# Kernel tuning notes

Measured on AMD Instinct MI355X. Metric: run time of the kernel, lower is better.

## Reference

```python
import jax, jax.numpy as jnp
import numpy as np

N_NODES = 20000   # atoms
N_EDGES = 300000  # directed edges within cutoff
N_TRIP = 500000   # triplets (k->j->i)
H = 128           # hidden_channels
NR = 6            # num_radial
NS = 7            # num_spherical
NB = 8            # num_bilinear
OUT = 128         # out_channels
NLAY = 3          # num_layers in OutputBlock
NOB = 2           # num_blocks + 1 output blocks


def _silu(v):
    return v * jax.nn.sigmoid(v)  # swish


def setup_inputs() -> dict:
    key = jax.random.key(0)
    ks = jax.random.split(key, 20)
    s = lambda fan: np.float32(1.0 / np.sqrt(fan))
    inp = {}
    inp["x"] = jax.random.normal(ks[0], (N_EDGES, H), jnp.float32)
    inp["rbf"] = jax.random.uniform(ks[1], (N_EDGES, NR), jnp.float32)
    inp["sbf"] = jax.random.uniform(ks[2], (N_TRIP, NS * NR), jnp.float32)
    inp["i"] = jax.random.randint(ks[3], (N_EDGES,), 0, N_NODES)
    inp["idx_kj"] = jax.random.randint(ks[4], (N_TRIP,), 0, N_EDGES)
    inp["idx_ji"] = jax.random.randint(ks[5], (N_TRIP,), 0, N_EDGES)
    # Interaction params (weights stored [in, out] so y = x @ W)
    inp["W_rbf"] = jax.random.normal(ks[6], (NR, H), jnp.float32) * s(NR)
    inp["W_sbf"] = jax.random.normal(ks[7], (NS * NR, NB), jnp.float32) * s(NS * NR)
    inp["W_kj"] = jax.random.normal(ks[8], (H, H), jnp.float32) * s(H)
    inp["b_kj"] = jnp.zeros((H,), jnp.float32)
    inp["W_ji"] = jax.random.normal(ks[9], (H, H), jnp.float32) * s(H)
    inp["b_ji"] = jnp.zeros((H,), jnp.float32)
    inp["W_bil"] = jax.random.normal(ks[10], (H, NB, H), jnp.float32) * np.float32(2.0 / H)
    inp["W_lin"] = jax.random.normal(ks[11], (H, H), jnp.float32) * s(H)
    inp["b_lin"] = jnp.zeros((H,), jnp.float32)
    # OutputBlock params, stacked over the NOB blocks
    inp["out_lin_rbf"] = jax.random.normal(ks[12], (NOB, NR, H), jnp.float32) * s(NR)
    inp["out_lins_W"] = jax.random.normal(ks[13], (NOB, NLAY, H, H), jnp.float32) * s(H)
    inp["out_lins_b"] = jnp.zeros((NOB, NLAY, H), jnp.float32)
    inp["out_lin"] = jax.random.normal(ks[14], (NOB, H, OUT), jnp.float32) * s(H)
    return inp


def _output_block(xe, rbf, i, lin_rbf, lins_W, lins_b, lin_out):
    # OutputBlock.forward: gate edge features by rbf projection, scatter to nodes
    g = (rbf @ lin_rbf) * xe              # [E, H]
    g = jax.ops.segment_sum(g, i, num_segments=N_NODES)  # [N, H]
    for li in range(NLAY):
        g = _silu(g @ lins_W[li] + lins_b[li])
    return g @ lin_out                    # [N, OUT]


def _interaction(x, rbf, sbf, idx_kj, idx_ji,
                 W_rbf, W_sbf, W_kj, b_kj, W_ji, b_ji, W_bil, W_lin, b_lin):
    r = rbf @ W_rbf                       # [E, H]
    sproj = sbf @ W_sbf                   # [T, NB]
    x_ji = _silu(x @ W_ji + b_ji)         # [E, H]
    x_kj = _silu(x @ W_kj + b_kj) * r     # [E, H]
    xg = x_kj[idx_kj]                     # [T, H] triplet gather
    # einsum('wj,wl,ijl->wi', sproj, xg, W_bil) without the [T, H, NB] blowup:
    # loop over the small fixed bilinear dim NB, accumulating [T, H]
    t = jnp.zeros((xg.shape[0], H), xg.dtype)
    for jb in range(NB):
        t = t + sproj[:, jb:jb + 1] * (xg @ W_bil[:, jb, :].T)
    agg = jax.ops.segment_sum(t, idx_ji, num_segments=N_EDGES)  # scatter to edges
    return _silu((x_ji + agg) @ W_lin + b_lin)


def reference(x, rbf, sbf, i, idx_kj, idx_ji,
              W_rbf, W_sbf, W_kj, b_kj, W_ji, b_ji, W_bil, W_lin, b_lin,
              out_lin_rbf, out_lins_W, out_lins_b, out_lin):
    P = _output_block(x, rbf, i, out_lin_rbf[0], out_lins_W[0], out_lins_b[0], out_lin[0])
    x2 = _interaction(x, rbf, sbf, idx_kj, idx_ji,
                      W_rbf, W_sbf, W_kj, b_kj, W_ji, b_ji, W_bil, W_lin, b_lin)
    P = P + _output_block(x2, rbf, i, out_lin_rbf[1], out_lins_W[1], out_lins_b[1], out_lin[1])
    return P.sum(axis=0)  # batch=None path: global readout [OUT]
```

## Files before the change

### kernel.cpp

```cpp
#include <hip/hip_runtime.h>
#include <hip/hip_fp16.h>

#define NN 20000
#define NE 300000
#define NT 500000
#define HD 128
#define NRR 6
#define NSNRD 42
#define NBB 8

using f16x8 = __attribute__((ext_vector_type(8))) _Float16;
using f32x4 = __attribute__((ext_vector_type(4))) float;

__device__ __forceinline__ float silu_f(float v){ return v / (1.f + __expf(-v)); }

__device__ __forceinline__ void pk_add(__half2* p, float lo, float hi){
  __half2 h = __floats2half2_rn(lo, hi);
  unsigned int b = *reinterpret_cast<unsigned int*>(&h);
  asm volatile("global_atomic_pk_add_f16 %0, %1, off" :: "v"(p), "v"(b) : "memory");
}

__device__ __forceinline__ void gload16(const void* g, char* lds_dst){
  __builtin_amdgcn_global_load_lds(
    (const __attribute__((address_space(1))) void*)g,
    (__attribute__((address_space(3))) void*)lds_dst, 16, 0, 0);
}

__global__ void k_x16(const float* __restrict__ x, __half* __restrict__ xh){
  long i = ((long)blockIdx.x*256 + threadIdx.x)*8;
  if(i < (long)NE*HD){
    float4 a = *(const float4*)(x+i), b = *(const float4*)(x+i+4);
    __half h8[8];
    h8[0]=__float2half(a.x); h8[1]=__float2half(a.y);
    h8[2]=__float2half(a.z); h8[3]=__float2half(a.w);
    h8[4]=__float2half(b.x); h8[5]=__float2half(b.y);
    h8[6]=__float2half(b.z); h8[7]=__float2half(b.w);
    *(float4*)(xh+i) = *(float4*)h8;
  }
}

__global__ void k_prep(const float* __restrict__ Wb, __half* __restrict__ WB2,
                       const float* __restrict__ Wkj, const float* __restrict__ Wji,
                       const float* __restrict__ Wlin, __half* __restrict__ WkjT,
                       __half* __restrict__ WjiT, __half* __restrict__ WlinT,
                       const float* __restrict__ olW, __half* __restrict__ wo6){
  int bid = blockIdx.x, tid = threadIdx.x;
  if(bid < 512){
    int idx = bid*256 + tid;
    int l = idx & 127, i = (idx>>7) & 127, jb = idx>>14;
    WB2[jb*16384 + i*128 + l] = __float2half(Wb[i*1024 + jb*128 + l]);
  } else if(bid < 704){
    int idx = (bid-512)*256 + tid;
    int which = idx>>14, rem = idx & 16383;
    int i = rem>>7, k = rem & 127;
    const float* src = which==0 ? Wkj : (which==1 ? Wji : Wlin);
    __half* dst = which==0 ? WkjT : (which==1 ? WjiT : WlinT);
    dst[rem] = __float2half(src[k*HD + i]);
  } else {
    int idx = (bid-704)*256 + tid;
    int lw = idx>>14, rem = idx & 16383;
    int i = rem>>7, k = rem & 127;
    wo6[lw*16384 + rem] = __float2half(olW[lw*16384 + k*HD + i]);
  }
}

#define EROWS 128
#define PRE_A 0
#define PRE_B 32768
#define PRE_RBF 65536
#define PRE_WR 68608
#define PRE_LS 71680
#define PRE_NID 74752
#define SH_PRE 75264
__global__ __launch_bounds__(512,4)
void k_edge_pre(const __half* __restrict__ xh, const float* __restrict__ rbf,
                const int* __restrict__ nid, const __half* __restrict__ WkjT,
                const float* __restrict__ bkj, const float* __restrict__ Wrbf,
                const float* __restrict__ lrbf0, __half* __restrict__ xkj,
                __half* __restrict__ g0){
  extern __shared__ char sm[];
  int tid = threadIdx.x;
  long e0 = (long)blockIdx.x * EROWS;
  for(int c=tid;c<2048;c+=512){
    int i=c>>4, cc=c&15;
    float4 v = *(const float4*)(WkjT + i*128 + cc*8);
    *(float4*)(sm + PRE_B + ((i*256+cc*16)^((i&7)<<4))) = v;
  }
  for(int c=tid;c<2048;c+=512){
    int r=c>>4, cc=c&15; long e=e0+r;
    float4 v = (e<NE) ? *(const float4*)(xh + e*HD + cc*8)
                      : (float4){0.f,0.f,0.f,0.f};
    *(float4*)(sm + PRE_A + ((r*256+cc*16)^((r&7)<<4))) = v;
  }
  float* rbft=(float*)(sm+PRE_RBF);
  for(int q=tid;q<EROWS*NRR;q+=512){ long e=e0+q/NRR; rbft[q]=(e<NE)? rbf[e*NRR + q%NRR] : 0.f; }
  float* wrbf=(float*)(sm+PRE_WR);
  for(int q=tid;q<NRR*HD;q+=512) wrbf[q]=Wrbf[q];
  float* ls0=(float*)(sm+PRE_LS);
  for(int q=tid;q<NRR*HD;q+=512) ls0[q]=lrbf0[q];
  int* nids=(int*)(sm+PRE_NID);
  if (tid < EROWS){ long e=e0+tid; nids[tid]=(e<NE)? nid[e] : 0; }
  __syncthreads();
  int lane=tid&63, wid=tid>>6, wr=wid>>1, wc=wid&1;
  f16x8 af[2][4];
  #pragma unroll
  for(int rt=0;rt<2;rt++){
    int r = wr*32 + rt*16 + (lane&15);
    #pragma unroll
    for(int ks=0;ks<4;ks++)
      af[rt][ks] = *(const f16x8*)(sm + PRE_A + ((r*256 + (ks*4+(lane>>4))*16)^((r&7)<<4)));
  }
  f32x4 acc[2][4];
  #pragma unroll
  for(int rt=0;rt<2;rt++){
    #pragma unroll
    for(int ct=0;ct<4;ct++) acc[rt][ct]=(f32x4){0.f,0.f,0.f,0.f};
  }
  #pragma unroll
  for(int ct=0;ct<4;ct++){
    int i = wc*64 + ct*16 + (lane&15);
    #pragma unroll
    for(int ks=0;ks<4;ks++){
      f16x8 b = *(const f16x8*)(sm + PRE_B + ((i*256 + (ks*4+(lane>>4))*16)^((i&7)<<4)));
      acc[0][ct] = __builtin_amdgcn_mfma_f32_16x16x32_f16(af[0][ks], b, acc[0][ct], 0,0,0);
      acc[1][ct] = __builtin_amdgcn_mfma_f32_16x16x32_f16(af[1][ks], b, acc[1][ct], 0,0,0);
    }
  }
  #pragma unroll
  for(int rt=0;rt<2;rt++){
    #pragma unroll
    for(int j=0;j<4;j++){
      int rloc = wr*32 + rt*16 + (lane>>4)*4 + j;
      long e = e0 + rloc;
      bool ok = (e<NE);
      int nb = nids[rloc];
      #pragma unroll
      for(int ct=0;ct<4;ct++){
        int h = wc*64 + ct*16 + (lane&15);
        float v = silu_f(acc[rt][ct][j] + bkj[h]);
        float r2=0.f, gate=0.f;
        #pragma unroll
        for(int q=0;q<NRR;q++){
          float rb = rbft[rloc*NRR+q];
          r2   += rb*wrbf[q*HD+h];
          gate += rb*ls0[q*HD+h];
        }
        float xval = __half2float(*(const __half*)(sm + PRE_A +
                       ((rloc*256 + (h>>3)*16)^((rloc&7)<<4)) + (h&7)*2));
        float w1 = v*r2;
        float w2 = gate*xval;
        float p1 = __shfl_xor(w1, 1, 64);
        float p2 = __shfl_xor(w2, 1, 64);
        if(ok && !(lane&1)){
          *(__half2*)(xkj + e*HD + h) = __floats2half2_rn(w1, p1);
          pk_add((__half2*)(g0 + (long)nb*HD + h), w2, p2);
        }
      }
    }
  }
}

#define TROWS 128
#define OFF_BUF 0
#define OFF_SP 49152
#define OFF_KJ 51200
#define OFF_JI 51712
#define OFF_WSB 52224
#define SH_TRIP 53568
__global__ __launch_bounds__(512,4)
void k_triplet_mfma(const __half* __restrict__ xkj, const float* __restrict__ sbf,
                    const float* __restrict__ Wsbf,
                    const int* __restrict__ ikj, const int* __restrict__ iji,
                    const __half* __restrict__ WB2, __half* __restrict__ agg){
  extern __shared__ char sm[];
  int tid = threadIdx.x;
  long t0 = (long)blockIdx.x * TROWS;
  int* kjs = (int*)(sm + OFF_KJ);
  int* jis = (int*)(sm + OFF_JI);
  if (tid < TROWS){
    int ok = (t0 + tid) < NT;
    kjs[tid] = ok ? ikj[t0+tid] : 0;
    jis[tid] = ok ? iji[t0+tid] : -1;
  }
  float* sbuf = (float*)(sm + OFF_BUF);
  for(int q=tid;q<TROWS*NSNRD;q+=512){
    long t = t0 + q/NSNRD;
    sbuf[q] = (t<NT) ? sbf[t*NSNRD + q%NSNRD] : 0.f;
  }
  float* wsb = (float*)(sm + OFF_WSB);
  for(int q=tid;q<NSNRD*NBB;q+=512) wsb[q]=Wsbf[q];
  __syncthreads();
  __half* spl = (__half*)(sm + OFF_SP);
  {
    int r = tid>>2, j0 = (tid&3)*2;
    float a0=0.f,a1=0.f;
    for(int q=0;q<NSNRD;q++){
      float v = sbuf[r*NSNRD+q];
      a0 += v*wsb[q*NBB+j0];
      a1 += v*wsb[q*NBB+j0+1];
    }
    spl[r*NBB+j0]=__float2half(a0); spl[r*NBB+j0+1]=__float2half(a1);
  }
  __syncthreads();
  for(int c=tid;c<TROWS*16;c+=512){
    int w = c>>4, cc = c&15;
    float4 v = *(const float4*)(xkj + (long)kjs[w]*HD + cc*8);
    *(float4*)(sm + OFF_BUF + ((w*256 + cc*16)^((w&7)<<4))) = v;
  }
  __syncthreads();
  int lane = tid & 63;
  int wid = tid>>6, wr = wid>>1, wc = wid&1;
  f16x8 au[2][4];
  #pragma unroll
  for(int rt=0;rt<2;rt++){
    int w = wr*32 + rt*16 + (lane&15);
    #pragma unroll
    for(int ks=0;ks<4;ks++)
      au[rt][ks] = *(const f16x8*)(sm + OFF_BUF + ((w*256 + ks*64 + (lane>>4)*16)^((w&7)<<4)));
  }
  __syncthreads();
  #pragma unroll
  for(int u=0;u<2;u++){
    int c = u*512 + tid;
    int i = c>>3, lc = (c&7) ^ (i&7);
    gload16(WB2 + i*128 + lc*8,
            sm + OFF_BUF + u*8192 + (tid>>6)*1024);
  }
  #pragma unroll
  for(int u=0;u<2;u++){
    int c = u*512 + tid;
    int i = c>>3, lc = (c&7) ^ (i&7);
    gload16(WB2 + i*128 + 64 + lc*8,
            sm + OFF_BUF + 16384 + u*8192 + (tid>>6)*1024);
  }
  f32x4 acc[2][4];
  #pragma unroll
  for(int rt=0;rt<2;rt++){
    #pragma unroll
    for(int ct=0;ct<4;ct++) acc[rt][ct] = (f32x4){0.f,0.f,0.f,0.f};
  }
  _Float16 sr[2];
  #pragma unroll
  for(int p=0;p<16;p++){
    int jb = p>>1, h = p&1;
    if(h==0){
      #pragma unroll
      for(int rt=0;rt<2;rt++)
        sr[rt] = *(const _Float16*)&spl[(wr*32 + rt*16 + (lane&15))*NBB + jb];
    }
    if(p<15) asm volatile("s_waitcnt vmcnt(2)" ::: "memory");
    else     asm volatile("s_waitcnt vmcnt(0)" ::: "memory");
    __builtin_amdgcn_s_barrier();
    asm volatile("" ::: "memory");
    if(p+2 < 16){
      int np = p+2, njb = np>>1, nh = np&1;
      #pragma unroll
      for(int u=0;u<2;u++){
        int c = u*512 + tid;
        int i = c>>3, lc = (c&7) ^ (i&7);
        gload16(WB2 + njb*16384 + i*128 + nh*64 + lc*8,
                sm + OFF_BUF + ((p+2)%3)*16384 + u*8192 + (tid>>6)*1024);
      }
    }
    const char* bbase = sm + OFF_BUF + (p%3)*16384;
    #pragma unroll
    for(int ksl=0;ksl<2;ksl++){
      int ks = h*2 + ksl;
      f16x8 as2[2];
      #pragma unroll
      for(int rt=0;rt<2;rt++){
        #pragma unroll
        for(int j=0;j<8;j++) as2[rt][j] = au[rt][ks][j]*sr[rt];
      }
      #pragma unroll
      for(int ct=0;ct<4;ct++){
        int it = wc*64 + ct*16 + (lane&15);
        int chunk = (ksl*4 + (lane>>4)) ^ (it&7);
        f16x8 b = *(const f16x8*)(bbase + it*128 + chunk*16);
        #pragma unroll
        for(int rt=0;rt<2;rt++)
          acc[rt][ct] = __builtin_amdgcn_mfma_f32_16x16x32_f16(as2[rt], b, acc[rt][ct], 0,0,0);
      }
    }
  }
  #pragma unroll
  for(int rt=0;rt<2;rt++){
    #pragma unroll
    for(int r=0;r<4;r++){
      int w = wr*32 + rt*16 + (lane>>4)*4 + r;
      int ji = jis[w];
      #pragma unroll
      for(int ct=0;ct<4;ct++){
        float v = acc[rt][ct][r];
        float p = __shfl_xor(v, 1, 64);
        if (ji >= 0 && !(lane&1))
          pk_add((__half2*)(agg + (long)ji*HD + wc*64 + ct*16 + (lane&15)), v, p);
      }
    }
  }
}

#define PO_A 0
#define PO_B 32768
#define PO_RBF 65536
#define PO_LS 68608
#define PO_NID 71680
#define SH_POST 72192
__global__ __launch_bounds__(512,4)
void k_edge_post(const __half* __restrict__ xh, const float* __restrict__ rbf,
                 const __half* __restrict__ aggh, const int* __restrict__ nid,
                 const __half* __restrict__ WjiT, const float* __restrict__ bji,
                 const __half* __restrict__ WlinT, const float* __restrict__ blin,
                 const float* __restrict__ lrbf1, __half* __restrict__ g1){
  extern __shared__ char sm[];
  int tid = threadIdx.x;
  long e0 = (long)blockIdx.x * EROWS;
  for(int c=tid;c<2048;c+=512){
    int i=c>>4, cc=c&15;
    float4 v = *(const float4*)(WjiT + i*128 + cc*8);
    *(float4*)(sm + PO_B + ((i*256+cc*16)^((i&7)<<4))) = v;
  }
  for(int c=tid;c<2048;c+=512){
    int r=c>>4, cc=c&15; long e=e0+r;
    float4 v = (e<NE) ? *(const float4*)(xh + e*HD + cc*8)
                      : (float4){0.f,0.f,0.f,0.f};
    *(float4*)(sm + PO_A + ((r*256+cc*16)^((r&7)<<4))) = v;
  }
  float* rbft=(float*)(sm+PO_RBF);
  for(int q=tid;q<EROWS*NRR;q+=512){ long e=e0+q/NRR; rbft[q]=(e<NE)? rbf[e*NRR + q%NRR] : 0.f; }
  float* ls1=(float*)(sm+PO_LS);
  for(int q=tid;q<NRR*HD;q+=512) ls1[q]=lrbf1[q];
  int* nids=(int*)(sm+PO_NID);
  if (tid < EROWS){ long e=e0+tid; nids[tid]=(e<NE)? nid[e] : 0; }
  __syncthreads();
  int lane=tid&63, wid=tid>>6, wr=wid>>1, wc=wid&1;
  f16x8 af[2][4];
  #pragma unroll
  for(int rt=0;rt<2;rt++){
    int r = wr*32 + rt*16 + (lane&15);
    #pragma unroll
    for(int ks=0;ks<4;ks++)
      af[rt][ks] = *(const f16x8*)(sm + PO_A + ((r*256 + (ks*4+(lane>>4))*16)^((r&7)<<4)));
  }
  f32x4 acc[2][4];
  #pragma unroll
  for(int rt=0;rt<2;rt++){
    #pragma unroll
    for(int ct=0;ct<4;ct++) acc[rt][ct]=(f32x4){0.f,0.f,0.f,0.f};
  }
  #pragma unroll
  for(int ct=0;ct<4;ct++){
    int i = wc*64 + ct*16 + (lane&15);
    #pragma unroll
    for(int ks=0;ks<4;ks++){
      f16x8 b = *(const f16x8*)(sm + PO_B + ((i*256 + (ks*4+(lane>>4))*16)^((i&7)<<4)));
      acc[0][ct] = __builtin_amdgcn_mfma_f32_16x16x32_f16(af[0][ks], b, acc[0][ct], 0,0,0);
      acc[1][ct] = __builtin_amdgcn_mfma_f32_16x16x32_f16(af[1][ks], b, acc[1][ct], 0,0,0);
    }
  }
  __syncthreads();
  #pragma unroll
  for(int rt=0;rt<2;rt++){
    #pragma unroll
    for(int j=0;j<4;j++){
      int rloc = wr*32 + rt*16 + (lane>>4)*4 + j;
      long e = e0 + rloc;
      #pragma unroll
      for(int ct=0;ct<4;ct++){
        int h = wc*64 + ct*16 + (lane&15);
        float v = silu_f(acc[rt][ct][j] + bji[h]);
        v += (e<NE) ? __half2float(aggh[e*HD + h]) : 0.f;
        int byo = ((rloc*256 + (h>>3)*16)^((rloc&7)<<4)) + (h&7)*2;
        *(__half*)(sm + PO_A + byo) = __float2half(v);
      }
    }
  }
  for(int c=tid;c<2048;c+=512){
    int i=c>>4, cc=c&15;
    float4 v = *(const float4*)(WlinT + i*128 + cc*8);
    *(float4*)(sm + PO_B + ((i*256+cc*16)^((i&7)<<4))) = v;
  }
  __syncthreads();
  f16x8 af2[2][4];
  #pragma unroll
  for(int rt=0;rt<2;rt++){
    int r = wr*32 + rt*16 + (lane&15);
    #pragma unroll
    for(int ks=0;ks<4;ks++)
      af2[rt][ks] = *(const f16x8*)(sm + PO_A + ((r*256 + (ks*4+(lane>>4))*16)^((r&7)<<4)));
  }
  f32x4 acc2[2][4];
  #pragma unroll
  for(int rt=0;rt<2;rt++){
    #pragma unroll
    for(int ct=0;ct<4;ct++) acc2[rt][ct]=(f32x4){0.f,0.f,0.f,0.f};
  }
  #pragma unroll
  for(int ct=0;ct<4;ct++){
    int i = wc*64 + ct*16 + (lane&15);
    #pragma unroll
    for(int ks=0;ks<4;ks++){
      f16x8 b = *(const f16x8*)(sm + PO_B + ((i*256 + (ks*4+(lane>>4))*16)^((i&7)<<4)));
      acc2[0][ct] = __builtin_amdgcn_mfma_f32_16x16x32_f16(af2[0][ks], b, acc2[0][ct], 0,0,0);
      acc2[1][ct] = __builtin_amdgcn_mfma_f32_16x16x32_f16(af2[1][ks], b, acc2[1][ct], 0,0,0);
    }
  }
  #pragma unroll
  for(int rt=0;rt<2;rt++){
    #pragma unroll
    for(int j=0;j<4;j++){
      int rloc = wr*32 + rt*16 + (lane>>4)*4 + j;
      long e = e0 + rloc;
      bool ok = (e<NE);
      int nb = nids[rloc];
      #pragma unroll
      for(int ct=0;ct<4;ct++){
        int h = wc*64 + ct*16 + (lane&15);
        float x2 = silu_f(acc2[rt][ct][j] + blin[h]);
        float gate = 0.f;
        #pragma unroll
        for(int q=0;q<NRR;q++) gate += rbft[rloc*NRR+q]*ls1[q*HD+h];
        float w = gate*x2;
        float p = __shfl_xor(w, 1, 64);
        if(ok && !(lane&1))
          pk_add((__half2*)(g1 + (long)nb*HD + h), w, p);
      }
    }
  }
}

#define SH_MLPC 65536
__global__ __launch_bounds__(512,4)
void k_mlp_chain(const __half* __restrict__ g0, const __half* __restrict__ g1,
                 const __half* __restrict__ wo6, const float* __restrict__ olb,
                 float* __restrict__ s0, float* __restrict__ s1){
  extern __shared__ char sm[];
  int tid = threadIdx.x;
  int nblk = (NN+EROWS-1)/EROWS;
  int which = blockIdx.x / nblk;
  long r0 = (long)(blockIdx.x % nblk) * EROWS;
  const __half* gin = which ? g1 : g0;
  float* s = which ? s1 : s0;
  for(int c=tid;c<2048;c+=512){
    int r=c>>4, cc=c&15; long rr=r0+r;
    float4 v;
    if(rr<NN) v = *(const float4*)(gin + rr*HD + cc*8);
    else      v = (float4){0.f,0.f,0.f,0.f};
    *(float4*)(sm + ((r*256+cc*16)^((r&7)<<4))) = v;
  }
  int lane=tid&63, wid=tid>>6, wr=wid>>1, wc=wid&1;
  for(int L=0; L<3; ++L){
    const __half* WT = wo6 + (which*3+L)*16384;
    const float* b   = olb + (which*3+L)*128;
    for(int c=tid;c<2048;c+=512){
      int i=c>>4, cc=c&15;
      float4 v = *(const float4*)(WT + i*128 + cc*8);
      *(float4*)(sm + 32768 + ((i*256+cc*16)^((i&7)<<4))) = v;
    }
    __syncthreads();
    f16x8 af[2][4];
    #pragma unroll
    for(int rt=0;rt<2;rt++){
      int r = wr*32 + rt*16 + (lane&15);
      #pragma unroll
      for(int ks=0;ks<4;ks++)
        af[rt][ks] = *(const f16x8*)(sm + ((r*256 + (ks*4+(lane>>4))*16)^((r&7)<<4)));
    }
    f32x4 acc[2][4];
    #pragma unroll
    for(int rt=0;rt<2;rt++){
      #pragma unroll
      for(int ct=0;ct<4;ct++) acc[rt][ct]=(f32x4){0.f,0.f,0.f,0.f};
    }
    #pragma unroll
    for(int ct=0;ct<4;ct++){
      int i = wc*64 + ct*16 + (lane&15);
      #pragma unroll
      for(int ks=0;ks<4;ks++){
        f16x8 bfr = *(const f16x8*)(sm + 32768 + ((i*256 + (ks*4+(lane>>4))*16)^((i&7)<<4)));
        acc[0][ct] = __builtin_amdgcn_mfma_f32_16x16x32_f16(af[0][ks], bfr, acc[0][ct], 0,0,0);
        acc[1][ct] = __builtin_amdgcn_mfma_f32_16x16x32_f16(af[1][ks], bfr, acc[1][ct], 0,0,0);
      }
    }
    __syncthreads();
    if(L < 2){
      #pragma unroll
      for(int rt=0;rt<2;rt++){
        #pragma unroll
        for(int j=0;j<4;j++){
          int rloc = wr*32 + rt*16 + (lane>>4)*4 + j;
          #pragma unroll
          for(int ct=0;ct<4;ct++){
            int h = wc*64 + ct*16 + (lane&15);
            float v = silu_f(acc[rt][ct][j] + b[h]);
            int byo = ((rloc*256 + (h>>3)*16)^((rloc&7)<<4)) + (h&7)*2;
            *(__half*)(sm + byo) = __float2half(v);
          }
        }
      }
    } else {
      float vsum[4];
      #pragma unroll
      for(int ct=0;ct<4;ct++) vsum[ct]=0.f;
      #pragma unroll
      for(int rt=0;rt<2;rt++){
        #pragma unroll
        for(int j=0;j<4;j++){
          int rloc = wr*32 + rt*16 + (lane>>4)*4 + j;
          long rr = r0 + rloc;
          #pragma unroll
          for(int ct=0;ct<4;ct++){
            int h = wc*64 + ct*16 + (lane&15);
            float v = (rr<NN) ? silu_f(acc[rt][ct][j] + b[h]) : 0.f;
            vsum[ct] += v;
          }
        }
      }
      #pragma unroll
      for(int ct=0;ct<4;ct++){
        vsum[ct] += __shfl_xor(vsum[ct], 16, 64);
        vsum[ct] += __shfl_xor(vsum[ct], 32, 64);
      }
      if((lane>>4)==0){
        #pragma unroll
        for(int ct=0;ct<4;ct++)
          atomicAdd(&s[wc*64 + ct*16 + (lane&15)], vsum[ct]);
      }
    }
  }
}

__global__ void k_readout(const float* __restrict__ s0, const float* __restrict__ s1,
                          const float* __restrict__ OL, float* __restrict__ out){
  int o = threadIdx.x;
  float acc=0.f;
  for(int h=0;h<HD;h++) acc += s0[h]*OL[h*HD+o] + s1[h]*OL[HD*HD + h*HD+o];
  out[o] = acc;
}

extern "C" void kernel_launch(void* const* d_in, const int* in_sizes, int n_in,
                              void* d_out, int out_size, void* d_ws, size_t ws_size,
                              hipStream_t stream) {
  const float* x     = (const float*)d_in[0];
  const float* rbf   = (const float*)d_in[1];
  const float* sbf   = (const float*)d_in[2];
  const int*   nid   = (const int*)d_in[3];
  const int*   ikj   = (const int*)d_in[4];
  const int*   iji   = (const int*)d_in[5];
  const float* W_rbf = (const float*)d_in[6];
  const float* W_sbf = (const float*)d_in[7];
  const float* W_kj  = (const float*)d_in[8];
  const float* b_kj  = (const float*)d_in[9];
  const float* W_ji  = (const float*)d_in[10];
  const float* b_ji  = (const float*)d_in[11];
  const float* W_bil = (const float*)d_in[12];
  const float* W_lin = (const float*)d_in[13];
  const float* b_lin = (const float*)d_in[14];
  const float* olrbf = (const float*)d_in[15];
  const float* olW   = (const float*)d_in[16];
  const float* olb   = (const float*)d_in[17];
  const float* olin  = (const float*)d_in[18];
  float* out = (float*)d_out;

  size_t off = 0;
  auto alloc = [&](size_t bytes)->size_t{ size_t r = off; off = (off + bytes + 255) & ~(size_t)255; return r; };
  size_t o_xkj  = alloc((size_t)NE*HD*2);
  size_t o_xh   = alloc((size_t)NE*HD*2);
  size_t o_agg  = alloc((size_t)NE*HD*2);
  size_t o_wb2  = alloc((size_t)NBB*HD*HD*2);
  size_t o_wkjT = alloc((size_t)HD*HD*2);
  size_t o_wjiT = alloc((size_t)HD*HD*2);
  size_t o_wlinT= alloc((size_t)HD*HD*2);
  size_t o_wo6  = alloc((size_t)6*HD*HD*2);
  size_t o_g0   = alloc((size_t)NN*HD*2);
  size_t o_g1   = alloc((size_t)NN*HD*2);
  size_t o_s0   = alloc(512);
  size_t o_s1   = alloc(512);
  if (off > ws_size) return;
  char* ws = (char*)d_ws;
  __half* xkj  = (__half*)(ws + o_xkj);
  __half* xh   = (__half*)(ws + o_xh);
  __half* agg  = (__half*)(ws + o_agg);
  __half* wb2  = (__half*)(ws + o_wb2);
  __half* wkjT = (__half*)(ws + o_wkjT);
  __half* wjiT = (__half*)(ws + o_wjiT);
  __half* wlinT= (__half*)(ws + o_wlinT);
  __half* wo6  = (__half*)(ws + o_wo6);
  __half* g0   = (__half*)(ws + o_g0);
  __half* g1   = (__half*)(ws + o_g1);
  float* s0    = (float*)(ws + o_s0);
  float* s1    = (float*)(ws + o_s1);

  hipFuncSetAttribute((const void*)k_edge_pre,     hipFuncAttributeMaxDynamicSharedMemorySize, SH_PRE);
  hipFuncSetAttribute((const void*)k_edge_post,    hipFuncAttributeMaxDynamicSharedMemorySize, SH_POST);
  hipFuncSetAttribute((const void*)k_triplet_mfma, hipFuncAttributeMaxDynamicSharedMemorySize, SH_TRIP);
  hipFuncSetAttribute((const void*)k_mlp_chain,    hipFuncAttributeMaxDynamicSharedMemorySize, SH_MLPC);

  hipMemsetAsync(agg, 0, (size_t)NE*HD*2, stream);
  hipMemsetAsync(g0,  0, (size_t)NN*HD*2, stream);
  hipMemsetAsync(g1,  0, (size_t)NN*HD*2, stream);
  hipMemsetAsync(s0,  0, 512, stream);
  hipMemsetAsync(s1,  0, 512, stream);

  k_x16<<<(int)(((long)NE*HD/8 + 255)/256),256,0,stream>>>(x, xh);
  k_prep<<<1088,256,0,stream>>>(W_bil, wb2, W_kj, W_ji, W_lin, wkjT, wjiT, wlinT, olW, wo6);

  k_edge_pre<<<(NE+EROWS-1)/EROWS,512,SH_PRE,stream>>>(xh, rbf, nid, wkjT, b_kj, W_rbf,
                                                       olrbf, xkj, g0);
  k_triplet_mfma<<<(NT+TROWS-1)/TROWS,512,SH_TRIP,stream>>>(xkj, sbf, W_sbf, ikj, iji, wb2, agg);
  k_edge_post<<<(NE+EROWS-1)/EROWS,512,SH_POST,stream>>>(xh, rbf, agg, nid, wjiT, b_ji,
                                                         wlinT, b_lin, olrbf + NRR*HD, g1);

  int mlpg = (NN+EROWS-1)/EROWS;
  k_mlp_chain<<<2*mlpg,512,SH_MLPC,stream>>>(g0, g1, wo6, olb, s0, s1);

  k_readout<<<1,128,0,stream>>>(s0, s1, olin, out);
}
```

Before: 736.7 us.

## Compute rbf projections with MFMA and load x tile directly from global

The two 6-wide rbf projections (r = rbf@W_rbf and gate = rbf@lin_rbf0) move from scalar FMA loops over LDS to fp16 MFMA, using K padded with zeros and fp16 copies of rbf and the weights staged in LDS. The x tile no longer goes through LDS: MFMA A fragments load straight from global memory, and the epilogue rereads x elements from global. This cuts LDS use and per-element scalar work, which may allow more resident blocks. It costs fp16 rounding of rbf and the weights, wasted MFMA work on the padded K, and scattered uncoalesced global reads of x in the epilogue.

New measurement: 763.6 us. +3.6%, slower.

```diff
diff --git a/kernel.cpp b/kernel.cpp
--- a/kernel.cpp
+++ b/kernel.cpp
@@ -65,13 +65,12 @@
 }
 
 #define EROWS 128
-#define PRE_A 0
-#define PRE_B 32768
-#define PRE_RBF 65536
-#define PRE_WR 68608
-#define PRE_LS 71680
-#define PRE_NID 74752
-#define SH_PRE 75264
+#define PRE_B 0
+#define PRE_RBF 32768
+#define PRE_WR 43008
+#define PRE_LS 53248
+#define PRE_NID 63488
+#define SH_PRE 64000
 __global__ __launch_bounds__(512,4)
 void k_edge_pre(const __half* __restrict__ xh, const float* __restrict__ rbf,
                 const int* __restrict__ nid, const __half* __restrict__ WkjT,
@@ -86,18 +85,18 @@
     float4 v = *(const float4*)(WkjT + i*128 + cc*8);
     *(float4*)(sm + PRE_B + ((i*256+cc*16)^((i&7)<<4))) = v;
   }
-  for(int c=tid;c<2048;c+=512){
-    int r=c>>4, cc=c&15; long e=e0+r;
-    float4 v = (e<NE) ? *(const float4*)(xh + e*HD + cc*8)
-                      : (float4){0.f,0.f,0.f,0.f};
-    *(float4*)(sm + PRE_A + ((r*256+cc*16)^((r&7)<<4))) = v;
-  }
-  float* rbft=(float*)(sm+PRE_RBF);
-  for(int q=tid;q<EROWS*NRR;q+=512){ long e=e0+q/NRR; rbft[q]=(e<NE)? rbf[e*NRR + q%NRR] : 0.f; }
-  float* wrbf=(float*)(sm+PRE_WR);
-  for(int q=tid;q<NRR*HD;q+=512) wrbf[q]=Wrbf[q];
-  float* ls0=(float*)(sm+PRE_LS);
-  for(int q=tid;q<NRR*HD;q+=512) ls0[q]=lrbf0[q];
+  __half* rbfp = (__half*)(sm + PRE_RBF);
+  for(int c=tid;c<4096;c+=512){
+    int r=c>>5, k=c&31; long e=e0+r;
+    rbfp[r*40+k] = (k<NRR && e<NE) ? __float2half(rbf[e*NRR+k]) : __float2half(0.f);
+  }
+  __half* wrt = (__half*)(sm + PRE_WR);
+  __half* lst = (__half*)(sm + PRE_LS);
+  for(int c=tid;c<4096;c+=512){
+    int i=c>>5, k=c&31;
+    wrt[i*40+k] = (k<NRR) ? __float2half(Wrbf[k*HD+i])  : __float2half(0.f);
+    lst[i*40+k] = (k<NRR) ? __float2half(lrbf0[k*HD+i]) : __float2half(0.f);
+  }
   int* nids=(int*)(sm+PRE_NID);
   if (tid < EROWS){ long e=e0+tid; nids[tid]=(e<NE)? nid[e] : 0; }
   __syncthreads();
@@ -105,16 +104,19 @@
   f16x8 af[2][4];
   #pragma unroll
   for(int rt=0;rt<2;rt++){
-    int r = wr*32 + rt*16 + (lane&15);
-    #pragma unroll
-    for(int ks=0;ks<4;ks++)
-      af[rt][ks] = *(const f16x8*)(sm + PRE_A + ((r*256 + (ks*4+(lane>>4))*16)^((r&7)<<4)));
-  }
-  f32x4 acc[2][4];
-  #pragma unroll
-  for(int rt=0;rt<2;rt++){
-    #pragma unroll
-    for(int ct=0;ct<4;ct++) acc[rt][ct]=(f32x4){0.f,0.f,0.f,0.f};
+    long e = e0 + wr*32 + rt*16 + (lane&15);
+    const __half* arow = xh + e*HD + (lane>>4)*8;
+    #pragma unroll
+    for(int ks=0;ks<4;ks++){
+      if(e<NE) af[rt][ks] = *(const f16x8*)(arow + ks*32);
+      else     af[rt][ks] = (f16x8){0,0,0,0,0,0,0,0};
+    }
+  }
+  f32x4 accM[2][4];
+  #pragma unroll
+  for(int rt=0;rt<2;rt++){
+    #pragma unroll
+    for(int ct=0;ct<4;ct++) accM[rt][ct]=(f32x4){0.f,0.f,0.f,0.f};
   }
   #pragma unroll
   for(int ct=0;ct<4;ct++){
@@ -122,8 +124,30 @@
     #pragma unroll
     for(int ks=0;ks<4;ks++){
       f16x8 b = *(const f16x8*)(sm + PRE_B + ((i*256 + (ks*4+(lane>>4))*16)^((i&7)<<4)));
-      acc[0][ct] = __builtin_amdgcn_mfma_f32_16x16x32_f16(af[0][ks], b, acc[0][ct], 0,0,0);
-      acc[1][ct] = __builtin_amdgcn_mfma_f32_16x16x32_f16(af[1][ks], b, acc[1][ct], 0,0,0);
+      accM[0][ct] = __builtin_amdgcn_mfma_f32_16x16x32_f16(af[0][ks], b, accM[0][ct], 0,0,0);
+      accM[1][ct] = __builtin_amdgcn_mfma_f32_16x16x32_f16(af[1][ks], b, accM[1][ct], 0,0,0);
+    }
+  }
+  f16x8 arf[2];
+  #pragma unroll
+  for(int rt=0;rt<2;rt++)
+    arf[rt] = *(const f16x8*)&rbfp[(wr*32 + rt*16 + (lane&15))*40 + (lane>>4)*8];
+  f32x4 accR[2][4], accG[2][4];
+  #pragma unroll
+  for(int rt=0;rt<2;rt++){
+    #pragma unroll
+    for(int ct=0;ct<4;ct++){ accR[rt][ct]=(f32x4){0.f,0.f,0.f,0.f};
+                             accG[rt][ct]=(f32x4){0.f,0.f,0.f,0.f}; }
+  }
+  #pragma unroll
+  for(int ct=0;ct<4;ct++){
+    int i = wc*64 + ct*16 + (lane&15);
+    f16x8 bw = *(const f16x8*)&wrt[i*40 + (lane>>4)*8];
+    f16x8 bl = *(const f16x8*)&lst[i*40 + (lane>>4)*8];
+    #pragma unroll
+    for(int rt=0;rt<2;rt++){
+      accR[rt][ct] = __builtin_amdgcn_mfma_f32_16x16x32_f16(arf[rt], bw, accR[rt][ct], 0,0,0);
+      accG[rt][ct] = __builtin_amdgcn_mfma_f32_16x16x32_f16(arf[rt], bl, accG[rt][ct], 0,0,0);
     }
   }
   #pragma unroll
@@ -137,18 +161,10 @@
       #pragma unroll
       for(int ct=0;ct<4;ct++){
         int h = wc*64 + ct*16 + (lane&15);
-        float v = silu_f(acc[rt][ct][j] + bkj[h]);
-        float r2=0.f, gate=0.f;
-        #pragma unroll
-        for(int q=0;q<NRR;q++){
-          float rb = rbft[rloc*NRR+q];
-          r2   += rb*wrbf[q*HD+h];
-          gate += rb*ls0[q*HD+h];
-        }
-        float xval = __half2float(*(const __half*)(sm + PRE_A +
-                       ((rloc*256 + (h>>3)*16)^((rloc&7)<<4)) + (h&7)*2));
-        float w1 = v*r2;
-        float w2 = gate*xval;
+        float v = silu_f(accM[rt][ct][j] + bkj[h]);
+        float xval = ok ? __half2float(xh[e*HD + h]) : 0.f;
+        float w1 = v*accR[rt][ct][j];
+        float w2 = accG[rt][ct][j]*xval;
         float p1 = __shfl_xor(w1, 1, 64);
         float p2 = __shfl_xor(w2, 1, 64);
         if(ok && !(lane&1)){
```
